# Kernel tuning notes

Measured on AMD Instinct MI355X. Metric: run time of the kernel, lower is better.

The kernel has to match this reference:

```python
import jax, jax.numpy as jnp
import numpy as np

EPS = 1e-06


def setup_inputs() -> dict:
    key = jax.random.key(0)
    k1, k2, k3 = jax.random.split(key, 3)
    N, L, H, D = 2, 2048, 8, 64
    return {
        "queries": jax.random.normal(k1, (N, L, H, D), dtype=jnp.float32),
        "keys": jax.random.normal(k2, (N, L, H, D), dtype=jnp.float32),
        "values": jax.random.normal(k3, (N, L, H, D), dtype=jnp.float32),
    }


def reference(queries, keys, values):
    # [N, L, H, D] -> [N, H, L, D]
    q = jnp.transpose(queries, (0, 2, 1, 3))
    k = jnp.transpose(keys, (0, 2, 1, 3))
    v = jnp.transpose(values, (0, 2, 1, 3))
    # kernel_method = sigmoid (applied to q and k only)
    q = jax.nn.sigmoid(q)
    k = jax.nn.sigmoid(k)
    L = q.shape[2]
    normal = (jnp.arange(L, dtype=q.dtype) + 1.0)[None, None, :]  # [1,1,L]

    sink_incoming = 1.0 / jnp.einsum('nhld,nhld->nhl', q + EPS, jnp.cumsum(k, axis=2) + EPS)
    source_outgoing = 1.0 / jnp.einsum('nhld,nhld->nhl', k + EPS, jnp.cumsum(q, axis=2) + EPS)
    sink_incoming = sink_incoming * normal
    source_outgoing = source_outgoing * normal

    conserved_sink = jnp.einsum(
        'nhld,nhld->nhl', q + EPS,
        jnp.cumsum(k * source_outgoing[..., None], axis=2) + EPS) / normal
    conserved_source = jnp.einsum(
        'nhld,nhld->nhl', k + EPS,
        jnp.cumsum(q * sink_incoming[..., None], axis=2) + EPS) / normal
    conserved_source = jnp.clip(conserved_source, -1.0, 1.0)

    sink_allocation = jax.nn.sigmoid(conserved_sink)
    conserved_source = jnp.exp(conserved_source)
    source_competition = conserved_source / jnp.cumsum(conserved_source, axis=-1) * normal

    # causal dot product: outer-product cumsum as in the original
    q_scaled = q * (sink_incoming / normal)[..., None]
    v_scaled = v * source_competition[..., None]
    kv = jnp.cumsum(jnp.einsum('nhld,nhlm->nhldm', k, v_scaled), axis=2)  # [N,H,L,D,M]
    qkv = jnp.einsum('nhld,nhldm->nhlm', q_scaled, kv)
    x = qkv * sink_allocation[..., None]
    # back to [N, L, H, M]
    return jnp.transpose(x, (0, 2, 1, 3))
```

## Files before the change

### kernel.cpp

```cpp
#include <hip/hip_runtime.h>
#include <math.h>

constexpr int Nn = 2, Hh = 8, Ll = 2048, Dd = 64;
constexpr int S  = Nn * Hh;
constexpr int C  = 64;
constexpr int NC = Ll / C;
constexpr int SC = S * NC;

constexpr int SB  = 72;
constexpr int SRP = 65;
constexpr int SS8 = 9;

#define EPSF 1e-6f

typedef __attribute__((ext_vector_type(8))) short short8;
typedef __attribute__((ext_vector_type(4))) float f32x4;
#define MFMA16(a, b, c) __builtin_amdgcn_mfma_f32_16x16x32_bf16(a, b, c, 0, 0, 0)

__device__ __forceinline__ float rcpf(float x) { return __builtin_amdgcn_rcpf(x); }
__device__ __forceinline__ float sigf(float x) { return rcpf(1.0f + __expf(-x)); }

__device__ __forceinline__ float waveRed(float v) {
#pragma unroll
    for (int off = 32; off > 0; off >>= 1) v += __shfl_xor(v, off, 64);
    return v;
}

__device__ __forceinline__ int gidx(int n, int l, int h, int d) {
    return ((n * Ll + l) * Hh + h) * Dd + d;
}

__device__ __forceinline__ float fc(const float4& v, int u) { return ((const float*)&v)[u]; }

__device__ __forceinline__ unsigned short f2bf(float x) {
    unsigned int u = __float_as_uint(x);
    unsigned int r = (u + 0x7fffu + ((u >> 16) & 1u)) >> 16;
    return (unsigned short)r;
}
__device__ __forceinline__ unsigned int pack2(float lo, float hi) {
    return (unsigned int)f2bf(lo) | ((unsigned int)f2bf(hi) << 16);
}
__device__ __forceinline__ float bf2f(unsigned short u) {
    return __uint_as_float(((unsigned int)u) << 16);
}
__device__ __forceinline__ float lo16(unsigned int x) { return __uint_as_float(x << 16); }
__device__ __forceinline__ float hi16(unsigned int x) { return __uint_as_float(x & 0xffff0000u); }
__device__ __forceinline__ void unpack8(const uint4& v, float* o) {
    o[0] = lo16(v.x); o[1] = hi16(v.x); o[2] = lo16(v.y); o[3] = hi16(v.y);
    o[4] = lo16(v.z); o[5] = hi16(v.z); o[6] = lo16(v.w); o[7] = hi16(v.w);
}

__global__ __launch_bounds__(256) void k_stage(const float* __restrict__ Q,
                                               const float* __restrict__ K,
                                               const float* __restrict__ V,
                                               unsigned short* __restrict__ Qb,
                                               unsigned short* __restrict__ Kb,
                                               unsigned short* __restrict__ Kt,
                                               unsigned short* __restrict__ Vt,
                                               float* __restrict__ SK,
                                               float* __restrict__ SQ) {
    __shared__ __align__(16) unsigned short skL[C * SB];
    __shared__ float scr[2048];
    int b = blockIdx.x, s = b / NC, c = b % NC;
    int n = s / Hh, h = s % Hh, t = threadIdx.x;
    int d0 = (4 * t) & 63, ig = t >> 4;
    size_t base = (size_t)b * 4096;
    float psk[4] = {0, 0, 0, 0}, psq[4] = {0, 0, 0, 0};
#pragma unroll
    for (int j = 0; j < 4; j++) {
        int i = ig + 16 * j;
        int id = gidx(n, c * C + i, h, d0);
        float4 q4 = *(const float4*)&Q[id];
        float4 k4 = *(const float4*)&K[id];
        float a0 = sigf(q4.x), a1 = sigf(q4.y), a2 = sigf(q4.z), a3 = sigf(q4.w);
        float b0 = sigf(k4.x), b1 = sigf(k4.y), b2 = sigf(k4.z), b3 = sigf(k4.w);
        uint2 pq2 = make_uint2(pack2(a0, a1), pack2(a2, a3));
        uint2 pk2 = make_uint2(pack2(b0, b1), pack2(b2, b3));
        *(uint2*)&Qb[base + i * 64 + d0] = pq2;
        *(uint2*)&Kb[base + i * 64 + d0] = pk2;
        *(uint2*)&skL[i * SB + d0] = pk2;
        psq[0] += a0; psq[1] += a1; psq[2] += a2; psq[3] += a3;
        psk[0] += b0; psk[1] += b1; psk[2] += b2; psk[3] += b3;
    }
#pragma unroll
    for (int r = 0; r < 4; r++) {
        scr[ig * 64 + d0 + r] = psk[r];
        scr[1024 + ig * 64 + d0 + r] = psq[r];
    }
    __syncthreads();
    if (t < 64) {
        float v = 0.f;
        for (int g = 0; g < 16; g++) v += scr[g * 64 + t];
        SK[b * 64 + t] = v;
    } else if (t < 128) {
        int d = t - 64; float v = 0.f;
        for (int g = 0; g < 16; g++) v += scr[1024 + g * 64 + d];
        SQ[b * 64 + d] = v;
    }
    {
        int i0 = (t & 15) * 4, dt = (t >> 4) * 4;
        uint2 kr[4]; float4 vr[4];
#pragma unroll
        for (int r = 0; r < 4; r++) {
            kr[r] = *(const uint2*)&skL[(i0 + r) * SB + dt];
            vr[r] = *(const float4*)&V[gidx(n, c * C + i0 + r, h, dt)];
        }
#pragma unroll
        for (int u = 0; u < 4; u++) {
            unsigned int e0 = (u < 2 ? kr[0].x : kr[0].y), e1 = (u < 2 ? kr[1].x : kr[1].y);
            unsigned int e2 = (u < 2 ? kr[2].x : kr[2].y), e3 = (u < 2 ? kr[3].x : kr[3].y);
            int sh = (u & 1) * 16;
            unsigned int lo = ((e0 >> sh) & 0xffffu) | (((e1 >> sh) & 0xffffu) << 16);
            unsigned int hi = ((e2 >> sh) & 0xffffu) | (((e3 >> sh) & 0xffffu) << 16);
            *(uint2*)&Kt[base + (dt + u) * 64 + i0] = make_uint2(lo, hi);
            *(uint2*)&Vt[base + (dt + u) * 64 + i0] = make_uint2(
                pack2(fc(vr[0], u), fc(vr[1], u)), pack2(fc(vr[2], u), fc(vr[3], u)));
        }
    }
}

__global__ __launch_bounds__(256) void k_pass1(const unsigned short* __restrict__ Qb,
                                               const unsigned short* __restrict__ Kb,
                                               const float* __restrict__ SK,
                                               const float* __restrict__ SQ,
                                               float* __restrict__ SKso,
                                               float* __restrict__ SQsi,
                                               float* __restrict__ si_g,
                                               float* __restrict__ rw1_g,
                                               float* __restrict__ rw2_g) {
    __shared__ __align__(16) unsigned short sqB[C * SB];
    __shared__ __align__(16) unsigned short skB[C * SB];
    __shared__ float P[C * SRP];
    __shared__ float scrA[C * SS8], scrB[C * SS8];
    __shared__ float colK[C], colQ[C], pk[Dd], pq[Dd], lsi[C], lso[C];
    int b = blockIdx.x, s = b / NC, c = b % NC, t = threadIdx.x;
    size_t base = (size_t)b * 4096;

#pragma unroll
    for (int j = 0; j < 2; j++) {
        int flat = 8 * t + 2048 * j, i = flat >> 6, d0 = flat & 63;
        uint4 xq = *(const uint4*)&Qb[base + flat];
        uint4 xk = *(const uint4*)&Kb[base + flat];
        *(uint4*)&sqB[i * SB + d0] = xq;
        *(uint4*)&skB[i * SB + d0] = xk;
        float qa[8], ka[8];
        unpack8(xq, qa); unpack8(xk, ka);
        float sq = 0.f, sk = 0.f;
#pragma unroll
        for (int u = 0; u < 8; u++) { sq += qa[u]; sk += ka[u]; }
        scrB[i * SS8 + (d0 >> 3)] = sq;
        scrA[i * SS8 + (d0 >> 3)] = sk;
    }
    {
        int d = t & 63, g = t >> 6;
        float pa = 0.f, pb = 0.f;
        for (int cp = g; cp < c; cp += 4) {
            pa += SK[(s * NC + cp) * 64 + d];
            pb += SQ[(s * NC + cp) * 64 + d];
        }
        P[2048 + g * 64 + d] = pa;
        P[2304 + g * 64 + d] = pb;
    }
    __syncthreads();
    if (t < 64) {
        float v = 0.f;
#pragma unroll
        for (int u = 0; u < 8; u++) v += scrA[t * SS8 + u];
        colK[t] = v;
    } else if (t < 128) {
        int i = t - 64; float v = 0.f;
#pragma unroll
        for (int u = 0; u < 8; u++) v += scrB[i * SS8 + u];
        colQ[i] = v;
    } else if (t < 192) {
        int d = t - 128;
        pk[d] = P[2048 + d] + P[2112 + d] + P[2176 + d] + P[2240 + d];
    } else {
        int d = t - 192;
        pq[d] = P[2304 + d] + P[2368 + d] + P[2432 + d] + P[2496 + d];
    }
    __syncthreads();

    {
        int w = t >> 6, lane = t & 63, m = lane & 15, q = lane >> 4;
        f32x4 acc[4] = {{0,0,0,0},{0,0,0,0},{0,0,0,0},{0,0,0,0}};
#pragma unroll
        for (int kk = 0; kk < 64; kk += 32) {
            short8 a = *(const short8*)&sqB[(16 * w + m) * SB + kk + q * 8];
#pragma unroll
            for (int J = 0; J < 4; J++) {
                short8 bb = *(const short8*)&skB[(16 * J + m) * SB + kk + q * 8];
                acc[J] = MFMA16(a, bb, acc[J]);
            }
        }
#pragma unroll
        for (int J = 0; J < 4; J++)
#pragma unroll
            for (int r = 0; r < 4; r++)
                P[(16 * w + 4 * q + r) * SRP + 16 * J + m] = acc[J][r];
    }
    __syncthreads();

    {
        int i = t >> 2, g = t & 3, l = c * C + i;
        float r1 = 0.f, r2 = 0.f;
        for (int jj = g; jj <= i; jj += 4) {
            r1 += P[i * SRP + jj] + EPSF * colK[jj];
            r2 += P[jj * SRP + i] + EPSF * colQ[jj];
        }
        float b1 = 0.f, b2 = 0.f;
#pragma unroll
        for (int u = 0; u < 16; u++) {
            int d = g * 16 + u;
            b1 += (bf2f(sqB[i * SB + d]) + EPSF) * (pk[d] + EPSF);
            b2 += (bf2f(skB[i * SB + d]) + EPSF) * (pq[d] + EPSF);
        }
        r1 += __shfl_xor(r1, 1, 64); r1 += __shfl_xor(r1, 2, 64);
        r2 += __shfl_xor(r2, 1, 64); r2 += __shfl_xor(r2, 2, 64);
        b1 += __shfl_xor(b1, 1, 64); b1 += __shfl_xor(b1, 2, 64);
        b2 += __shfl_xor(b2, 1, 64); b2 += __shfl_xor(b2, 2, 64);
        if (g == 0) {
            float nf = (float)(l + 1);
            float siF = nf * rcpf(b1 + r1), soF = nf * rcpf(b2 + r2);
            si_g[s * Ll + l] = siF;
            lsi[i] = siF; lso[i] = soF;
        }
    }
    __syncthreads();

    {
        int i = t >> 2, g = t & 3;
        float a1 = 0.f, a2 = 0.f;
        for (int jj = g; jj <= i; jj += 4) {
            a1 += lso[jj] * (P[i * SRP + jj] + EPSF * colK[jj]);
            a2 += lsi[jj] * (P[jj * SRP + i] + EPSF * colQ[jj]);
        }
        a1 += __shfl_xor(a1, 1, 64); a1 += __shfl_xor(a1, 2, 64);
        a2 += __shfl_xor(a2, 1, 64); a2 += __shfl_xor(a2, 2, 64);
        if (g == 0) {
            rw1_g[s * Ll + c * C + i] = a1;
            rw2_g[s * Ll + c * C + i] = a2;
        }
    }
    {
        int d = t >> 2, g = t & 3;
        float v1 = 0.f, v2 = 0.f;
#pragma unroll
        for (int u = 0; u < 16; u++) {
            int i = g * 16 + u;
            v1 += bf2f(skB[i * SB + d]) * lso[i];
            v2 += bf2f(sqB[i * SB + d]) * lsi[i];
        }
        v1 += __shfl_xor(v1, 1, 64); v1 += __shfl_xor(v1, 2, 64);
        v2 += __shfl_xor(v2, 1, 64); v2 += __shfl_xor(v2, 2, 64);
        if (g == 0) {
            SKso[b * 64 + d] = v1;
            SQsi[b * 64 + d] = v2;
        }
    }
}

__global__ __launch_bounds__(256) void k_pass2(const unsigned short* __restrict__ Qb,
                                               const unsigned short* __restrict__ Kb,
                                               const float* __restrict__ SKso,
                                               const float* __restrict__ SQsi,
                                               const float* __restrict__ si_g,
                                               const float* __restrict__ rw1_g,
                                               const float* __restrict__ rw2_g,
                                               float* __restrict__ s2_g,
                                               float* __restrict__ e_g,
                                               float* __restrict__ ecum_g,
                                               float* __restrict__ Tcs) {
    __shared__ float scr[512];
    __shared__ float pks[Dd], pqs[Dd], le[C];
    int b = blockIdx.x, s = b / NC, c = b % NC, t = threadIdx.x;

    {
        int d = t & 63, g = t >> 6;
        float pa = 0.f, pb = 0.f;
        for (int cp = g; cp < c; cp += 4) {
            pa += SKso[(s * NC + cp) * 64 + d];
            pb += SQsi[(s * NC + cp) * 64 + d];
        }
        scr[g * 64 + d] = pa;
        scr[256 + g * 64 + d] = pb;
    }
    __syncthreads();
    if (t < 64) pks[t] = scr[t] + scr[64 + t] + scr[128 + t] + scr[192 + t];
    else if (t < 128) {
        int d = t - 64;
        pqs[d] = scr[256 + d] + scr[320 + d] + scr[384 + d] + scr[448 + d];
    }
    __syncthreads();

    int i = t >> 2, g = t & 3, l = c * C + i;
    float b1 = 0.f, b2 = 0.f;
    size_t base = (size_t)b * 4096 + i * 64 + g * 16;
#pragma unroll
    for (int j = 0; j < 2; j++) {
        uint4 xq = *(const uint4*)&Qb[base + 8 * j];
        uint4 xk = *(const uint4*)&Kb[base + 8 * j];
        float qa[8], ka[8];
        unpack8(xq, qa); unpack8(xk, ka);
        int d = g * 16 + 8 * j;
#pragma unroll
        for (int u = 0; u < 8; u++) {
            b1 += (qa[u] + EPSF) * (pks[d + u] + EPSF);
            b2 += (ka[u] + EPSF) * (pqs[d + u] + EPSF);
        }
    }
    b1 += __shfl_xor(b1, 1, 64); b1 += __shfl_xor(b1, 2, 64);
    b2 += __shfl_xor(b2, 1, 64); b2 += __shfl_xor(b2, 2, 64);
    if (g == 0) {
        float nf = (float)(l + 1);
        float cs  = (b1 + rw1_g[s * Ll + l]) * rcpf(nf);
        float csr = (b2 + rw2_g[s * Ll + l]) * rcpf(nf);
        csr = fminf(fmaxf(csr, -1.f), 1.f);
        float e = __expf(csr);
        float sal = sigf(cs);
        s2_g[s * Ll + l] = si_g[s * Ll + l] * rcpf(nf) * sal;
        e_g[s * Ll + l] = e;
        le[i] = e;
    }
    __syncthreads();
    if (t < 64) {
        float run = le[t];
#pragma unroll
        for (int off = 1; off < 64; off <<= 1) {
            float o = __shfl_up(run, off, 64);
            if (t >= off) run += o;
        }
        ecum_g[s * Ll + c * C + t] = run;
        if (t == 63) Tcs[b] = run;
    }
}

__global__ __launch_bounds__(256) void k_kv(const unsigned short* __restrict__ Kt,
                                            const unsigned short* __restrict__ Vt,
                                            const float* __restrict__ e_g,
                                            const float* __restrict__ ecum_g,
                                            const float* __restrict__ Tcs,
                                            float* __restrict__ scomp_g,
                                            float* __restrict__ KVT) {
    __shared__ __align__(16) unsigned short skT[C * SB];
    __shared__ __align__(16) unsigned short vsT[C * SB];
    __shared__ float lsc[C];
    __shared__ float pcsv;
    int b = blockIdx.x, s = b / NC, c = b % NC, t = threadIdx.x;
    if (t < 64) {
        float v = (t < c) ? Tcs[s * NC + t] : 0.f;
        v = waveRed(v);
        if (t == 0) pcsv = v;
    }
    __syncthreads();
    if (t < 64) {
        int l = c * C + t;
        float ls = e_g[s * Ll + l] * rcpf(pcsv + ecum_g[s * Ll + l]) * (float)(l + 1);
        lsc[t] = ls;
        scomp_g[s * Ll + l] = ls;
    }
    __syncthreads();

    size_t base = (size_t)b * 4096;
#pragma unroll
    for (int j = 0; j < 2; j++) {
        int flat = 8 * t + 2048 * j, dR = flat >> 6, i0 = flat & 63;
        *(uint4*)&skT[dR * SB + i0] = *(const uint4*)&Kt[base + flat];
        uint4 vv = *(const uint4*)&Vt[base + flat];
        float x[8];
        unpack8(vv, x);
#pragma unroll
        for (int u = 0; u < 8; u++) x[u] *= lsc[i0 + u];
        uint4 o;
        o.x = pack2(x[0], x[1]); o.y = pack2(x[2], x[3]);
        o.z = pack2(x[4], x[5]); o.w = pack2(x[6], x[7]);
        *(uint4*)&vsT[dR * SB + i0] = o;
    }
    __syncthreads();

    {
        int w = t >> 6, lane = t & 63, m = lane & 15, q = lane >> 4;
        f32x4 acc[4] = {{0,0,0,0},{0,0,0,0},{0,0,0,0},{0,0,0,0}};
#pragma unroll
        for (int kk = 0; kk < 64; kk += 32) {
            short8 a = *(const short8*)&vsT[(16 * w + m) * SB + kk + q * 8];
#pragma unroll
            for (int J = 0; J < 4; J++) {
                short8 bb = *(const short8*)&skT[(16 * J + m) * SB + kk + q * 8];
                acc[J] = MFMA16(a, bb, acc[J]);
            }
        }
#pragma unroll
        for (int J = 0; J < 4; J++)
#pragma unroll
            for (int r = 0; r < 4; r++)
                KVT[(size_t)b * 4096 + (16 * w + 4 * q + r) * 64 + 16 * J + m] = acc[J][r];
    }
}

__global__ __launch_bounds__(256) void k_final(const unsigned short* __restrict__ Qb,
                                               const unsigned short* __restrict__ Kb,
                                               const unsigned short* __restrict__ Vt,
                                               const float* __restrict__ s2_g,
                                               const float* __restrict__ scomp_g,
                                               const float* __restrict__ KVT,
                                               float* __restrict__ Out) {
    __shared__ __align__(16) unsigned short sqB[C * SB];
    __shared__ __align__(16) unsigned short skB[C * SB];
    __shared__ __align__(16) unsigned short vsT[C * SB];
    __shared__ __align__(16) unsigned short stB[C * SB];
    __shared__ float lsc[C], s2l[C];
    int bb = blockIdx.x, s = bb / NC;
    int c = NC - 1 - (bb % NC);
    int b = s * NC + c;
    int n = s / Hh, h = s % Hh, t = threadIdx.x;
    int w = t >> 6, lane = t & 63, mf = lane & 15, qq = lane >> 4;
    int I0 = 16 * w;

    if (t < 64) lsc[t] = scomp_g[s * Ll + c * C + t];
    else if (t < 128) s2l[t - 64] = s2_g[s * Ll + c * C + (t - 64)];

    float4 kvr[4] = {make_float4(0.f, 0.f, 0.f, 0.f), make_float4(0.f, 0.f, 0.f, 0.f),
                     make_float4(0.f, 0.f, 0.f, 0.f), make_float4(0.f, 0.f, 0.f, 0.f)};
    for (int cp = 0; cp < c; cp++) {
        const float* Kp = &KVT[(size_t)(s * NC + cp) * 4096];
#pragma unroll
        for (int j = 0; j < 4; j++) {
            float4 x = *(const float4*)&Kp[4 * t + 1024 * j];
            kvr[j].x += x.x; kvr[j].y += x.y; kvr[j].z += x.z; kvr[j].w += x.w;
        }
    }

    size_t base = (size_t)b * 4096;
#pragma unroll
    for (int j = 0; j < 2; j++) {
        int flat = 8 * t + 2048 * j, i = flat >> 6, d0 = flat & 63;
        *(uint4*)&sqB[i * SB + d0] = *(const uint4*)&Qb[base + flat];
        *(uint4*)&skB[i * SB + d0] = *(const uint4*)&Kb[base + flat];
        *(uint4*)&vsT[i * SB + d0] = *(const uint4*)&Vt[base + flat];
    }
    __syncthreads();

    {
        f32x4 acc[4] = {{0,0,0,0},{0,0,0,0},{0,0,0,0},{0,0,0,0}};
#pragma unroll
        for (int kk = 0; kk < 64; kk += 32) {
            short8 a = *(const short8*)&sqB[(I0 + mf) * SB + kk + qq * 8];
#pragma unroll
            for (int J = 0; J < 4; J++) {
                short8 bb2 = *(const short8*)&skB[(16 * J + mf) * SB + kk + qq * 8];
                acc[J] = MFMA16(a, bb2, acc[J]);
            }
        }
#pragma unroll
        for (int J = 0; J < 4; J++)
#pragma unroll
            for (int r = 0; r < 4; r++) {
                int i = I0 + 4 * qq + r, jj = 16 * J + mf;
                float v = (jj <= i) ? acc[J][r] * lsc[jj] : 0.f;
                stB[i * SB + jj] = f2bf(v);
            }
    }
    __syncthreads();

#pragma unroll
    for (int j = 0; j < 4; j++) {
        int flat = 4 * t + 1024 * j, i = flat >> 6, d0 = flat & 63;
        *(uint2*)&skB[i * SB + d0] = make_uint2(pack2(kvr[j].x, kvr[j].y),
                                                pack2(kvr[j].z, kvr[j].w));
    }
    __syncthreads();

    f32x4 acc[4] = {{0,0,0,0},{0,0,0,0},{0,0,0,0},{0,0,0,0}};
#pragma unroll
    for (int kk = 0; kk < 64; kk += 32) {
        short8 a1 = *(const short8*)&sqB[(I0 + mf) * SB + kk + qq * 8];
        short8 a2 = *(const short8*)&stB[(I0 + mf) * SB + kk + qq * 8];
#pragma unroll
        for (int J = 0; J < 4; J++) {
            short8 b1 = *(const short8*)&skB[(16 * J + mf) * SB + kk + qq * 8];
            acc[J] = MFMA16(a1, b1, acc[J]);
            short8 b2 = *(const short8*)&vsT[(16 * J + mf) * SB + kk + qq * 8];
            acc[J] = MFMA16(a2, b2, acc[J]);
        }
    }
#pragma unroll
    for (int J = 0; J < 4; J++)
#pragma unroll
        for (int r = 0; r < 4; r++) {
            int io = I0 + 4 * qq + r;
            Out[gidx(n, c * C + io, h, 16 * J + mf)] = acc[J][r] * s2l[io];
        }
}

extern "C" void kernel_launch(void* const* d_in, const int* in_sizes, int n_in,
                              void* d_out, int out_size, void* d_ws, size_t ws_size,
                              hipStream_t stream) {
    const float* Q = (const float*)d_in[0];
    const float* K = (const float*)d_in[1];
    const float* V = (const float*)d_in[2];
    float* Out = (float*)d_out;

    float* ws    = (float*)d_ws;
    float* SK    = ws;
    float* SQ    = SK    + SC * 64;
    float* SKso  = SQ    + SC * 64;
    float* SQsi  = SKso  + SC * 64;
    float* si_g  = SQsi  + SC * 64;
    float* rw1_g = si_g  + S * Ll;
    float* rw2_g = rw1_g + S * Ll;
    float* s2_g  = rw2_g + S * Ll;
    float* e_g   = s2_g  + S * Ll;
    float* ecum_g= e_g   + S * Ll;
    float* scomp = ecum_g+ S * Ll;
    float* Tcs   = scomp + S * Ll;
    float* KVT   = Tcs   + SC;
    unsigned short* Qb = (unsigned short*)(KVT + (size_t)SC * 4096);
    unsigned short* Kb = Qb + (size_t)SC * 4096;
    unsigned short* Kt = Kb + (size_t)SC * 4096;
    unsigned short* Vt = Kt + (size_t)SC * 4096;

    k_stage<<<SC, 256, 0, stream>>>(Q, K, V, Qb, Kb, Kt, Vt, SK, SQ);
    k_pass1<<<SC, 256, 0, stream>>>(Qb, Kb, SK, SQ, SKso, SQsi, si_g, rw1_g, rw2_g);
    k_pass2<<<SC, 256, 0, stream>>>(Qb, Kb, SKso, SQsi, si_g, rw1_g, rw2_g, s2_g, e_g, ecum_g, Tcs);
    k_kv<<<SC, 256, 0, stream>>>(Kt, Vt, e_g, ecum_g, Tcs, scomp, KVT);
    k_final<<<SC, 256, 0, stream>>>(Qb, Kb, Vt, s2_g, scomp, KVT, Out);
}
```

Baseline: 111.7 us.

## Precompute exclusive KV prefix sums in a dedicated kernel; transpose K in LDS

Adds a k_prefixKV kernel that computes the exclusive prefix over chunks of the per-chunk KV outer products once and stores it as bf16. k_final then loads a single precomputed prefix instead of summing up to 31 fp32 KV tiles per block, which was quadratic in chunk count and load-imbalanced. The K transpose moves from k_stage (global Kt buffer) into k_kv via LDS, saving a global write and read. This costs an extra kernel launch and extra traffic for the bf16 prefix buffer, and the block ordering in k_final is no longer reversed.

```diff
diff --git a/kernel.cpp b/kernel.cpp
--- a/kernel.cpp
+++ b/kernel.cpp
@@ -55,11 +55,9 @@
                                                const float* __restrict__ V,
                                                unsigned short* __restrict__ Qb,
                                                unsigned short* __restrict__ Kb,
-                                               unsigned short* __restrict__ Kt,
                                                unsigned short* __restrict__ Vt,
                                                float* __restrict__ SK,
                                                float* __restrict__ SQ) {
-    __shared__ __align__(16) unsigned short skL[C * SB];
     __shared__ float scr[2048];
     int b = blockIdx.x, s = b / NC, c = b % NC;
     int n = s / Hh, h = s % Hh, t = threadIdx.x;
@@ -74,11 +72,8 @@
         float4 k4 = *(const float4*)&K[id];
         float a0 = sigf(q4.x), a1 = sigf(q4.y), a2 = sigf(q4.z), a3 = sigf(q4.w);
         float b0 = sigf(k4.x), b1 = sigf(k4.y), b2 = sigf(k4.z), b3 = sigf(k4.w);
-        uint2 pq2 = make_uint2(pack2(a0, a1), pack2(a2, a3));
-        uint2 pk2 = make_uint2(pack2(b0, b1), pack2(b2, b3));
-        *(uint2*)&Qb[base + i * 64 + d0] = pq2;
-        *(uint2*)&Kb[base + i * 64 + d0] = pk2;
-        *(uint2*)&skL[i * SB + d0] = pk2;
+        *(uint2*)&Qb[base + i * 64 + d0] = make_uint2(pack2(a0, a1), pack2(a2, a3));
+        *(uint2*)&Kb[base + i * 64 + d0] = make_uint2(pack2(b0, b1), pack2(b2, b3));
         psq[0] += a0; psq[1] += a1; psq[2] += a2; psq[3] += a3;
         psk[0] += b0; psk[1] += b1; psk[2] += b2; psk[3] += b3;
     }
@@ -99,23 +94,14 @@
     }
     {
         int i0 = (t & 15) * 4, dt = (t >> 4) * 4;
-        uint2 kr[4]; float4 vr[4];
-#pragma unroll
-        for (int r = 0; r < 4; r++) {
-            kr[r] = *(const uint2*)&skL[(i0 + r) * SB + dt];
+        float4 vr[4];
+#pragma unroll
+        for (int r = 0; r < 4; r++)
             vr[r] = *(const float4*)&V[gidx(n, c * C + i0 + r, h, dt)];
-        }
-#pragma unroll
-        for (int u = 0; u < 4; u++) {
-            unsigned int e0 = (u < 2 ? kr[0].x : kr[0].y), e1 = (u < 2 ? kr[1].x : kr[1].y);
-            unsigned int e2 = (u < 2 ? kr[2].x : kr[2].y), e3 = (u < 2 ? kr[3].x : kr[3].y);
-            int sh = (u & 1) * 16;
-            unsigned int lo = ((e0 >> sh) & 0xffffu) | (((e1 >> sh) & 0xffffu) << 16);
-            unsigned int hi = ((e2 >> sh) & 0xffffu) | (((e3 >> sh) & 0xffffu) << 16);
-            *(uint2*)&Kt[base + (dt + u) * 64 + i0] = make_uint2(lo, hi);
+#pragma unroll
+        for (int u = 0; u < 4; u++)
             *(uint2*)&Vt[base + (dt + u) * 64 + i0] = make_uint2(
                 pack2(fc(vr[0], u), fc(vr[1], u)), pack2(fc(vr[2], u), fc(vr[3], u)));
-        }
     }
 }
 
@@ -335,18 +321,26 @@
     }
 }
 
-__global__ __launch_bounds__(256) void k_kv(const unsigned short* __restrict__ Kt,
+__global__ __launch_bounds__(256) void k_kv(const unsigned short* __restrict__ Kb,
                                             const unsigned short* __restrict__ Vt,
                                             const float* __restrict__ e_g,
                                             const float* __restrict__ ecum_g,
                                             const float* __restrict__ Tcs,
                                             float* __restrict__ scomp_g,
                                             float* __restrict__ KVT) {
+    __shared__ __align__(16) unsigned short skL[C * SB];
     __shared__ __align__(16) unsigned short skT[C * SB];
     __shared__ __align__(16) unsigned short vsT[C * SB];
     __shared__ float lsc[C];
     __shared__ float pcsv;
     int b = blockIdx.x, s = b / NC, c = b % NC, t = threadIdx.x;
+    size_t base = (size_t)b * 4096;
+
+#pragma unroll
+    for (int j = 0; j < 2; j++) {
+        int flat = 8 * t + 2048 * j, i = flat >> 6, d0 = flat & 63;
+        *(uint4*)&skL[i * SB + d0] = *(const uint4*)&Kb[base + flat];
+    }
     if (t < 64) {
         float v = (t < c) ? Tcs[s * NC + t] : 0.f;
         v = waveRed(v);
@@ -361,11 +355,9 @@
     }
     __syncthreads();
 
-    size_t base = (size_t)b * 4096;
 #pragma unroll
     for (int j = 0; j < 2; j++) {
         int flat = 8 * t + 2048 * j, dR = flat >> 6, i0 = flat & 63;
-        *(uint4*)&skT[dR * SB + i0] = *(const uint4*)&Kt[base + flat];
         uint4 vv = *(const uint4*)&Vt[base + flat];
         float x[8];
         unpack8(vv, x);
@@ -376,6 +368,21 @@
         o.z = pack2(x[4], x[5]); o.w = pack2(x[6], x[7]);
         *(uint4*)&vsT[dR * SB + i0] = o;
     }
+    {
+        int i0 = (t & 15) * 4, dt = (t >> 4) * 4;
+        uint2 kr[4];
+#pragma unroll
+        for (int r = 0; r < 4; r++) kr[r] = *(const uint2*)&skL[(i0 + r) * SB + dt];
+#pragma unroll
+        for (int u = 0; u < 4; u++) {
+            unsigned int e0 = (u < 2 ? kr[0].x : kr[0].y), e1 = (u < 2 ? kr[1].x : kr[1].y);
+            unsigned int e2 = (u < 2 ? kr[2].x : kr[2].y), e3 = (u < 2 ? kr[3].x : kr[3].y);
+            int sh = (u & 1) * 16;
+            unsigned int lo = ((e0 >> sh) & 0xffffu) | (((e1 >> sh) & 0xffffu) << 16);
+            unsigned int hi = ((e2 >> sh) & 0xffffu) | (((e3 >> sh) & 0xffffu) << 16);
+            *(uint2*)&skT[(dt + u) * SB + i0] = make_uint2(lo, hi);
+        }
+    }
     __syncthreads();
 
     {
@@ -395,6 +402,22 @@
 #pragma unroll
             for (int r = 0; r < 4; r++)
                 KVT[(size_t)b * 4096 + (16 * w + 4 * q + r) * 64 + 16 * J + m] = acc[J][r];
+    }
+}
+
+__global__ __launch_bounds__(256) void k_prefixKV(const float* __restrict__ KVT,
+                                                  unsigned short* __restrict__ KVpb) {
+    int bx = blockIdx.x, s = bx >> 3, sub = bx & 7;
+    int e0 = sub * 512 + 2 * threadIdx.x;
+    float2 x[NC];
+#pragma unroll
+    for (int cp = 0; cp < NC; cp++)
+        x[cp] = *(const float2*)&KVT[(size_t)(s * NC + cp) * 4096 + e0];
+    float r0 = 0.f, r1 = 0.f;
+#pragma unroll
+    for (int cp = 0; cp < NC; cp++) {
+        *(unsigned int*)&KVpb[(size_t)(s * NC + cp) * 4096 + e0] = pack2(r0, r1);
+        r0 += x[cp].x; r1 += x[cp].y;
     }
 }
 
@@ -403,16 +426,14 @@
                                                const unsigned short* __restrict__ Vt,
                                                const float* __restrict__ s2_g,
                                                const float* __restrict__ scomp_g,
-                                               const float* __restrict__ KVT,
+                                               const unsigned short* __restrict__ KVpb,
                                                float* __restrict__ Out) {
     __shared__ __align__(16) unsigned short sqB[C * SB];
     __shared__ __align__(16) unsigned short skB[C * SB];
     __shared__ __align__(16) unsigned short vsT[C * SB];
     __shared__ __align__(16) unsigned short stB[C * SB];
     __shared__ float lsc[C], s2l[C];
-    int bb = blockIdx.x, s = bb / NC;
-    int c = NC - 1 - (bb % NC);
-    int b = s * NC + c;
+    int b = blockIdx.x, s = b / NC, c = b % NC;
     int n = s / Hh, h = s % Hh, t = threadIdx.x;
     int w = t >> 6, lane = t & 63, mf = lane & 15, qq = lane >> 4;
     int I0 = 16 * w;
@@ -420,18 +441,12 @@
     if (t < 64) lsc[t] = scomp_g[s * Ll + c * C + t];
     else if (t < 128) s2l[t - 64] = s2_g[s * Ll + c * C + (t - 64)];
 
-    float4 kvr[4] = {make_float4(0.f, 0.f, 0.f, 0.f), make_float4(0.f, 0.f, 0.f, 0.f),
-                     make_float4(0.f, 0.f, 0.f, 0.f), make_float4(0.f, 0.f, 0.f, 0.f)};
-    for (int cp = 0; cp < c; cp++) {
-        const float* Kp = &KVT[(size_t)(s * NC + cp) * 4096];
-#pragma unroll
-        for (int j = 0; j < 4; j++) {
-            float4 x = *(const float4*)&Kp[4 * t + 1024 * j];
-            kvr[j].x += x.x; kvr[j].y += x.y; kvr[j].z += x.z; kvr[j].w += x.w;
-        }
-    }
-
     size_t base = (size_t)b * 4096;
+    uint4 kvp[2];
+#pragma unroll
+    for (int j = 0; j < 2; j++)
+        kvp[j] = *(const uint4*)&KVpb[base + 8 * t + 2048 * j];
+
 #pragma unroll
     for (int j = 0; j < 2; j++) {
         int flat = 8 * t + 2048 * j, i = flat >> 6, d0 = flat & 63;
@@ -464,10 +479,9 @@
     __syncthreads();
 
 #pragma unroll
-    for (int j = 0; j < 4; j++) {
-        int flat = 4 * t + 1024 * j, i = flat >> 6, d0 = flat & 63;
-        *(uint2*)&skB[i * SB + d0] = make_uint2(pack2(kvr[j].x, kvr[j].y),
-                                                pack2(kvr[j].z, kvr[j].w));
+    for (int j = 0; j < 2; j++) {
+        int flat = 8 * t + 2048 * j, i = flat >> 6, d0 = flat & 63;
+        *(uint4*)&skB[i * SB + d0] = kvp[j];
     }
     __syncthreads();
 
@@ -515,14 +529,15 @@
     float* scomp = ecum_g+ S * Ll;
     float* Tcs   = scomp + S * Ll;
     float* KVT   = Tcs   + SC;
-    unsigned short* Qb = (unsigned short*)(KVT + (size_t)SC * 4096);
-    unsigned short* Kb = Qb + (size_t)SC * 4096;
-    unsigned short* Kt = Kb + (size_t)SC * 4096;
-    unsigned short* Vt = Kt + (size_t)SC * 4096;
-
-    k_stage<<<SC, 256, 0, stream>>>(Q, K, V, Qb, Kb, Kt, Vt, SK, SQ);
+    unsigned short* Qb   = (unsigned short*)(KVT + (size_t)SC * 4096);
+    unsigned short* Kb   = Qb   + (size_t)SC * 4096;
+    unsigned short* Vt   = Kb   + (size_t)SC * 4096;
+    unsigned short* KVpb = Vt   + (size_t)SC * 4096;
+
+    k_stage<<<SC, 256, 0, stream>>>(Q, K, V, Qb, Kb, Vt, SK, SQ);
     k_pass1<<<SC, 256, 0, stream>>>(Qb, Kb, SK, SQ, SKso, SQsi, si_g, rw1_g, rw2_g);
     k_pass2<<<SC, 256, 0, stream>>>(Qb, Kb, SKso, SQsi, si_g, rw1_g, rw2_g, s2_g, e_g, ecum_g, Tcs);
-    k_kv<<<SC, 256, 0, stream>>>(Kt, Vt, e_g, ecum_g, Tcs, scomp, KVT);
-    k_final<<<SC, 256, 0, stream>>>(Qb, Kb, Vt, s2_g, scomp, KVT, Out);
-}
+    k_kv<<<SC, 256, 0, stream>>>(Kb, Vt, e_g, ecum_g, Tcs, scomp, KVT);
+    k_prefixKV<<<128, 256, 0, stream>>>(KVT, KVpb);
+    k_final<<<SC, 256, 0, stream>>>(Qb, Kb, Vt, s2_g, scomp, KVpb, Out);
+}
```

Result: faster. 105.8 us (-5.3%).
